# Kernel optimization log

Measured on AMD Instinct MI355X. Metric: run time of the kernel, lower is better.

The kernel has to match this reference:

```python
import jax, jax.numpy as jnp
import numpy as np

B, S, D = 16, 4096, 64
DROPOUT_KEY = jax.random.key(1)


def setup_inputs() -> dict:
    key = jax.random.key(0)
    kq, kk, kv = jax.random.split(key, 3)
    return {
        "query": jax.random.normal(kq, (B, S, D), dtype=jnp.float32),
        "key": jax.random.normal(kk, (B, S, D), dtype=jnp.float32),
        "value": jax.random.normal(kv, (B, S, D), dtype=jnp.float32),
        "dropout_p": jnp.float32(0.01),
        "inv_scale_factor": jnp.float32(8.0),  # sqrt(head_dim)
    }


def reference(query, key, value, dropout_p, inv_scale_factor):
    # scores: [B, Sq, Skv]
    scores = jnp.einsum("bqd,bkd->bqk", query, key) / inv_scale_factor
    attn = jax.nn.softmax(scores, axis=-1)
    # deterministic dropout with a fixed key (faithful train-mode dropout)
    keep = jax.random.bernoulli(DROPOUT_KEY, 1.0 - dropout_p, attn.shape)
    attn = jnp.where(keep, attn / (1.0 - dropout_p), 0.0)
    return jnp.einsum("bqk,bkd->bqd", attn, value)
```

## Files before the change

kernel.cpp:

```cpp
#include <hip/hip_runtime.h>
#include <stdint.h>


typedef _Float16 half4 __attribute__((ext_vector_type(4)));
typedef _Float16 half8 __attribute__((ext_vector_type(8)));
typedef float    f32x4 __attribute__((ext_vector_type(4)));

#if defined(__has_builtin)
#if __has_builtin(__builtin_amdgcn_exp2f)
#define EXP2(x) __builtin_amdgcn_exp2f(x)
#else
#define EXP2(x) exp2f(x)
#endif
#else
#define EXP2(x) exp2f(x)
#endif

#define ROTL(x, r) __builtin_amdgcn_alignbit((x), (x), 32 - (r))

__device__ __forceinline__ uint32_t tf2x32_xor(uint32_t n) {
  const uint32_t ks2 = 0x1BD11BDBu;
  uint32_t x0 = 0u, x1 = n;
#define TFR(r) { x0 += x1; x1 = ROTL(x1, r); x1 ^= x0; }
  x1 += 1u;
  TFR(13) TFR(15) TFR(26) TFR(6)
  x0 += 1u;  x1 += ks2 + 1u;
  TFR(17) TFR(29) TFR(16) TFR(24)
  x0 += ks2; x1 += 2u;
  TFR(13) TFR(15) TFR(26) TFR(6)
  x1 += 4u;
  TFR(17) TFR(29) TFR(16) TFR(24)
  x0 += 1u;  x1 += ks2 + 4u;
  TFR(13) TFR(15) TFR(26) TFR(6)
  x0 += ks2; x1 += 5u;
#undef TFR
  return x0 ^ x1;
}


__global__ void cvt_qk_kernel(const float* __restrict__ q,
                              const float* __restrict__ k,
                              const float* __restrict__ inv_scale,
                              _Float16* __restrict__ qh,
                              _Float16* __restrict__ kh) {
  const int tid = blockIdx.x * 256 + threadIdx.x;
  const int half_t = 1048576;
  const float qs = 1.4426950408889634f / inv_scale[0];
  if (tid < half_t) {
    float4 d = *(const float4*)(q + (size_t)tid * 4);
    half4 h = { (_Float16)(d.x * qs), (_Float16)(d.y * qs),
                (_Float16)(d.z * qs), (_Float16)(d.w * qs) };
    *(half4*)(qh + (size_t)tid * 4) = h;
  } else {
    const int t2 = tid - half_t;
    float4 d = *(const float4*)(k + (size_t)t2 * 4);
    half4 h = { (_Float16)d.x, (_Float16)d.y, (_Float16)d.z, (_Float16)d.w };
    *(half4*)(kh + (size_t)t2 * 4) = h;
  }
}

__global__ void cvt_v_kernel(const float* __restrict__ v,
                             _Float16* __restrict__ vt) {
  __shared__ float tile[64][65];
  const int b  = blockIdx.x >> 6;
  const int st = blockIdx.x & 63;
  const int t  = threadIdx.x;
  const float* src = v + ((size_t)b * 4096 + (size_t)st * 64) * 64;
#pragma unroll
  for (int i = 0; i < 4; ++i) {
    const int r = i * 16 + (t >> 4);
    const int c = (t & 15) * 4;
    float4 d = *(const float4*)(src + r * 64 + c);
    tile[r][c] = d.x; tile[r][c + 1] = d.y; tile[r][c + 2] = d.z; tile[r][c + 3] = d.w;
  }
  __syncthreads();
  _Float16* dst = vt + (size_t)b * 64 * 4096 + (size_t)st * 64;
#pragma unroll
  for (int i = 0; i < 4; ++i) {
    const int d0 = i * 16 + (t >> 4);
    const int s0 = (t & 15) * 4;
    half4 h = { (_Float16)tile[s0][d0],     (_Float16)tile[s0 + 1][d0],
                (_Float16)tile[s0 + 2][d0], (_Float16)tile[s0 + 3][d0] };
    *(half4*)(dst + (size_t)d0 * 4096 + s0) = h;
  }
}

__global__ __launch_bounds__(256, 4) void flash_attn(
    const _Float16* __restrict__ qh,
    const _Float16* __restrict__ kh,
    const _Float16* __restrict__ vth,
    const float* __restrict__ dropout_p,
    float* __restrict__ out) {
  __shared__ alignas(16) _Float16 Kt[2][64 * 72];
  __shared__ alignas(16) _Float16 Vt[2][64 * 72];

  const int pair = blockIdx.x & 7;
  const int q0   = (blockIdx.x >> 3) * 32;
  const int wave = threadIdx.x >> 6;
  const int lane = threadIdx.x & 63;
  const int l15  = lane & 15;
  const int l4   = lane >> 4;
  const int b2   = wave & 1;
  const int qw   = (wave >> 1) * 16;
  const int batch = pair + 8 * b2;

  const float keep_p = 1.0f - dropout_p[0];
  const uint32_t thr = (uint32_t)ceilf(keep_p * 8388608.0f);
  const uint32_t thr9 = (thr >= 8388608u) ? 0xFFFFFFFFu : (thr << 9);

  const _Float16* qp = qh +
      (((size_t)batch * 4096 + q0 + qw + l15) * 64 + l4 * 8);
  const half8 qfrag0 = *(const half8*)qp;
  const half8 qfrag1 = *(const half8*)(qp + 32);

  const f32x4 Zv = {0.f, 0.f, 0.f, 0.f};
  f32x4 oacc[4] = {Zv, Zv, Zv, Zv};
  float lpart = 0.f;

  const uint32_t nlo = ((uint32_t)batch << 24) +
                       ((uint32_t)(q0 + qw + l15) << 12) +
                       (uint32_t)(4 * l4);

  for (int step = 0; step < 64; ++step) {
    const int key0 = step * 64;
    __syncthreads();
#pragma unroll
    for (int bb = 0; bb < 2; ++bb) {
      const _Float16* kb = kh + ((size_t)(pair + 8 * bb) * 4096 + key0) * 64;
      const _Float16* vb = vth + (size_t)(pair + 8 * bb) * 64 * 4096 + key0;
#pragma unroll
      for (int i = 0; i < 2; ++i) {
        const int chunk = threadIdx.x + i * 256;
        const int row = chunk >> 3;
        const int c   = (chunk & 7) * 8;
        *(half8*)&Kt[bb][row * 72 + c] = *(const half8*)(kb + row * 64 + c);
        *(half8*)&Vt[bb][row * 72 + c] = *(const half8*)(vb + (size_t)row * 4096 + c);
      }
    }
    __syncthreads();

    f32x4 sacc[4];
#pragma unroll
    for (int t = 0; t < 4; ++t) {
      const half8 kf0 = *(const half8*)&Kt[b2][(16 * t + l15) * 72 + l4 * 8];
      const half8 kf1 = *(const half8*)&Kt[b2][(16 * t + l15) * 72 + l4 * 8 + 32];
      sacc[t] = __builtin_amdgcn_mfma_f32_16x16x32_f16(kf0, qfrag0, Zv, 0, 0, 0);
      sacc[t] = __builtin_amdgcn_mfma_f32_16x16x32_f16(kf1, qfrag1, sacc[t], 0, 0, 0);
    }

#pragma unroll
    for (int t = 0; t < 4; ++t) {
      const uint32_t cb = nlo + (uint32_t)(key0 + 16 * t);
      half4 pf;
#pragma unroll
      for (int r = 0; r < 4; ++r) {
        const uint32_t w = tf2x32_xor(cb + (uint32_t)r);
        const float p = EXP2(sacc[t][r]);
        lpart += p;
        pf[r] = (_Float16)((w < thr9) ? p : 0.0f);
      }
#pragma unroll
      for (int t2 = 0; t2 < 4; ++t2) {
        const half4 vf = *(const half4*)&Vt[b2][(16 * t2 + l15) * 72 + 16 * t + 4 * l4];
        oacc[t2] = __builtin_amdgcn_mfma_f32_16x16x16f16(pf, vf, oacc[t2], 0, 0, 0);
      }
    }
  }

  float l = lpart;
  l += __shfl_xor(l, 16, 64);
  l += __shfl_xor(l, 32, 64);
  float inv[4];
#pragma unroll
  for (int r = 0; r < 4; ++r)
    inv[r] = 1.0f / (keep_p * __shfl(l, 4 * l4 + r, 64));
#pragma unroll
  for (int t2 = 0; t2 < 4; ++t2)
#pragma unroll
    for (int r = 0; r < 4; ++r)
      out[((size_t)batch * 4096 + q0 + qw + 4 * l4 + r) * 64 + 16 * t2 + l15] =
          oacc[t2][r] * inv[r];
}


extern "C" void kernel_launch(void* const* d_in, const int* in_sizes, int n_in,
                              void* d_out, int out_size, void* d_ws, size_t ws_size,
                              hipStream_t stream) {
  const float* q   = (const float*)d_in[0];
  const float* k   = (const float*)d_in[1];
  const float* v   = (const float*)d_in[2];
  const float* dp  = (const float*)d_in[3];
  const float* isf = (const float*)d_in[4];
  float* out = (float*)d_out;

  const size_t N = (size_t)16 * 4096 * 64;
  _Float16* qh  = (_Float16*)d_ws;
  _Float16* kh  = qh + N;
  _Float16* vth = kh + N;

  cvt_qk_kernel<<<8192, 256, 0, stream>>>(q, k, isf, qh, kh);
  cvt_v_kernel<<<1024, 256, 0, stream>>>(v, vth);
  flash_attn<<<1024, 256, 0, stream>>>(qh, kh, vth, dp, out);
}
```

Before: 625.6 us.

## Precompute dropout mask as bitmask in separate kernel, read bits in attention

Adds a separate kernel that evaluates the Threefry hash once per attention element and packs keep decisions into 64-bit ballot words, 32 MB in total. The attention kernel then reads one mask word per row and step and applies it with shift and AND instead of running the hash inline. The hash also drops its first, trivial round. A fused fallback is kept for when the workspace is too small. The trade is extra mask memory traffic and one more kernel launch against removing hash ALU work from the MFMA loop.

```diff
diff --git a/kernel.cpp b/kernel.cpp
--- a/kernel.cpp
+++ b/kernel.cpp
@@ -18,12 +18,12 @@
 
 #define ROTL(x, r) __builtin_amdgcn_alignbit((x), (x), 32 - (r))
 
-__device__ __forceinline__ uint32_t tf2x32_xor(uint32_t n) {
+__device__ __forceinline__ uint32_t tf_hash(uint32_t x1) {
   const uint32_t ks2 = 0x1BD11BDBu;
-  uint32_t x0 = 0u, x1 = n;
+  uint32_t x0 = x1;
 #define TFR(r) { x0 += x1; x1 = ROTL(x1, r); x1 ^= x0; }
-  x1 += 1u;
-  TFR(13) TFR(15) TFR(26) TFR(6)
+  x1 = ROTL(x1, 13); x1 ^= x0;
+  TFR(15) TFR(26) TFR(6)
   x0 += 1u;  x1 += ks2 + 1u;
   TFR(17) TFR(29) TFR(16) TFR(24)
   x0 += ks2; x1 += 2u;
@@ -35,6 +35,38 @@
   x0 += ks2; x1 += 5u;
 #undef TFR
   return x0 ^ x1;
+}
+
+__device__ __forceinline__ uint32_t tf2x32_xor(uint32_t n) {
+  return tf_hash(n + 1u);
+}
+
+__device__ __forceinline__ uint32_t thr9_from(float keep_p) {
+  const uint32_t thr = (uint32_t)ceilf(keep_p * 8388608.0f);
+  return (thr >= 8388608u) ? 0xFFFFFFFFu : (thr << 9);
+}
+
+__global__ __launch_bounds__(256, 8) void prng_mask_kernel(
+    const float* __restrict__ dropout_p,
+    uint64_t* __restrict__ mask) {
+  const int lane = threadIdx.x & 63;
+  const uint32_t wid = (uint32_t)((blockIdx.x * 256 + threadIdx.x) >> 6);
+  const uint32_t thr9 = thr9_from(1.0f - dropout_p[0]);
+
+  const uint32_t base0 = (uint32_t)lane + 1u;
+  for (int it = 0; it < 128; ++it) {
+    const uint32_t g  = wid * 128u + (uint32_t)it;
+    const uint32_t nb = g * 256u + base0;
+    unsigned long long b0, b1, b2, b3;
+    b0 = __ballot(tf_hash(nb)         < thr9);
+    b1 = __ballot(tf_hash(nb + 64u)   < thr9);
+    b2 = __ballot(tf_hash(nb + 128u)  < thr9);
+    b3 = __ballot(tf_hash(nb + 192u)  < thr9);
+    if (lane == 0) {
+      uint64_t* p = mask + (size_t)g * 4;
+      p[0] = b0; p[1] = b1; p[2] = b2; p[3] = b3;
+    }
+  }
 }
 
 
@@ -89,6 +121,7 @@
     const _Float16* __restrict__ qh,
     const _Float16* __restrict__ kh,
     const _Float16* __restrict__ vth,
+    const uint64_t* __restrict__ mask,
     const float* __restrict__ dropout_p,
     float* __restrict__ out) {
   __shared__ alignas(16) _Float16 Kt[2][64 * 72];
@@ -103,26 +136,31 @@
   const int b2   = wave & 1;
   const int qw   = (wave >> 1) * 16;
   const int batch = pair + 8 * b2;
+  const int qrow  = q0 + qw + l15;
 
   const float keep_p = 1.0f - dropout_p[0];
-  const uint32_t thr = (uint32_t)ceilf(keep_p * 8388608.0f);
-  const uint32_t thr9 = (thr >= 8388608u) ? 0xFFFFFFFFu : (thr << 9);
-
-  const _Float16* qp = qh +
-      (((size_t)batch * 4096 + q0 + qw + l15) * 64 + l4 * 8);
+
+  const _Float16* qp = qh + (((size_t)batch * 4096 + qrow) * 64 + l4 * 8);
   const half8 qfrag0 = *(const half8*)qp;
   const half8 qfrag1 = *(const half8*)(qp + 32);
+
+  const uint64_t* mrow = mask + (((size_t)batch << 18) + ((size_t)qrow << 6));
+
+  int shl[2][4];
+#pragma unroll
+  for (int tt = 0; tt < 2; ++tt)
+#pragma unroll
+    for (int r = 0; r < 4; ++r) shl[tt][r] = 31 - 16 * tt - 4 * l4 - r;
 
   const f32x4 Zv = {0.f, 0.f, 0.f, 0.f};
   f32x4 oacc[4] = {Zv, Zv, Zv, Zv};
   float lpart = 0.f;
 
-  const uint32_t nlo = ((uint32_t)batch << 24) +
-                       ((uint32_t)(q0 + qw + l15) << 12) +
-                       (uint32_t)(4 * l4);
-
   for (int step = 0; step < 64; ++step) {
     const int key0 = step * 64;
+    const uint64_t mword = mrow[step];
+    const uint32_t mlo = (uint32_t)mword;
+    const uint32_t mhi = (uint32_t)(mword >> 32);
     __syncthreads();
 #pragma unroll
     for (int bb = 0; bb < 2; ++bb) {
@@ -150,6 +188,90 @@
 
 #pragma unroll
     for (int t = 0; t < 4; ++t) {
+      const uint32_t mh = (t & 2) ? mhi : mlo;
+      half4 pf;
+#pragma unroll
+      for (int r = 0; r < 4; ++r) {
+        const float p = EXP2(sacc[t][r]);
+        lpart += p;
+        const uint32_t km = (uint32_t)(((int32_t)(mh << shl[t & 1][r])) >> 31);
+        pf[r] = (_Float16)__uint_as_float(__float_as_uint(p) & km);
+      }
+#pragma unroll
+      for (int t2 = 0; t2 < 4; ++t2) {
+        const half4 vf = *(const half4*)&Vt[b2][(16 * t2 + l15) * 72 + 16 * t + 4 * l4];
+        oacc[t2] = __builtin_amdgcn_mfma_f32_16x16x16f16(pf, vf, oacc[t2], 0, 0, 0);
+      }
+    }
+  }
+
+  float l = lpart;
+  l += __shfl_xor(l, 16, 64);
+  l += __shfl_xor(l, 32, 64);
+  float inv[4];
+#pragma unroll
+  for (int r = 0; r < 4; ++r)
+    inv[r] = 1.0f / (keep_p * __shfl(l, 4 * l4 + r, 64));
+#pragma unroll
+  for (int t2 = 0; t2 < 4; ++t2)
+#pragma unroll
+    for (int r = 0; r < 4; ++r)
+      out[((size_t)batch * 4096 + q0 + qw + 4 * l4 + r) * 64 + 16 * t2 + l15] =
+          oacc[t2][r] * inv[r];
+}
+
+__global__ __launch_bounds__(256, 4) void flash_attn_fused(
+    const _Float16* __restrict__ qh, const _Float16* __restrict__ kh,
+    const _Float16* __restrict__ vth, const float* __restrict__ dropout_p,
+    float* __restrict__ out) {
+  __shared__ alignas(16) _Float16 Kt[2][64 * 72];
+  __shared__ alignas(16) _Float16 Vt[2][64 * 72];
+  const int pair = blockIdx.x & 7;
+  const int q0   = (blockIdx.x >> 3) * 32;
+  const int wave = threadIdx.x >> 6;
+  const int lane = threadIdx.x & 63;
+  const int l15  = lane & 15;
+  const int l4   = lane >> 4;
+  const int b2   = wave & 1;
+  const int qw   = (wave >> 1) * 16;
+  const int batch = pair + 8 * b2;
+  const float keep_p = 1.0f - dropout_p[0];
+  const uint32_t thr9 = thr9_from(keep_p);
+  const _Float16* qp = qh + (((size_t)batch * 4096 + q0 + qw + l15) * 64 + l4 * 8);
+  const half8 qfrag0 = *(const half8*)qp;
+  const half8 qfrag1 = *(const half8*)(qp + 32);
+  const f32x4 Zv = {0.f, 0.f, 0.f, 0.f};
+  f32x4 oacc[4] = {Zv, Zv, Zv, Zv};
+  float lpart = 0.f;
+  const uint32_t nlo = ((uint32_t)batch << 24) +
+                       ((uint32_t)(q0 + qw + l15) << 12) + (uint32_t)(4 * l4);
+  for (int step = 0; step < 64; ++step) {
+    const int key0 = step * 64;
+    __syncthreads();
+#pragma unroll
+    for (int bb = 0; bb < 2; ++bb) {
+      const _Float16* kb = kh + ((size_t)(pair + 8 * bb) * 4096 + key0) * 64;
+      const _Float16* vb = vth + (size_t)(pair + 8 * bb) * 64 * 4096 + key0;
+#pragma unroll
+      for (int i = 0; i < 2; ++i) {
+        const int chunk = threadIdx.x + i * 256;
+        const int row = chunk >> 3;
+        const int c   = (chunk & 7) * 8;
+        *(half8*)&Kt[bb][row * 72 + c] = *(const half8*)(kb + row * 64 + c);
+        *(half8*)&Vt[bb][row * 72 + c] = *(const half8*)(vb + (size_t)row * 4096 + c);
+      }
+    }
+    __syncthreads();
+    f32x4 sacc[4];
+#pragma unroll
+    for (int t = 0; t < 4; ++t) {
+      const half8 kf0 = *(const half8*)&Kt[b2][(16 * t + l15) * 72 + l4 * 8];
+      const half8 kf1 = *(const half8*)&Kt[b2][(16 * t + l15) * 72 + l4 * 8 + 32];
+      sacc[t] = __builtin_amdgcn_mfma_f32_16x16x32_f16(kf0, qfrag0, Zv, 0, 0, 0);
+      sacc[t] = __builtin_amdgcn_mfma_f32_16x16x32_f16(kf1, qfrag1, sacc[t], 0, 0, 0);
+    }
+#pragma unroll
+    for (int t = 0; t < 4; ++t) {
       const uint32_t cb = nlo + (uint32_t)(key0 + 16 * t);
       half4 pf;
 #pragma unroll
@@ -166,7 +288,6 @@
       }
     }
   }
-
   float l = lpart;
   l += __shfl_xor(l, 16, 64);
   l += __shfl_xor(l, 32, 64);
@@ -197,8 +318,15 @@
   _Float16* qh  = (_Float16*)d_ws;
   _Float16* kh  = qh + N;
   _Float16* vth = kh + N;
+  uint64_t* mask = (uint64_t*)((char*)d_ws + 3 * N * sizeof(_Float16));
+  const size_t need = 3 * N * sizeof(_Float16) + ((size_t)1 << 25);
 
   cvt_qk_kernel<<<8192, 256, 0, stream>>>(q, k, isf, qh, kh);
   cvt_v_kernel<<<1024, 256, 0, stream>>>(v, vth);
-  flash_attn<<<1024, 256, 0, stream>>>(qh, kh, vth, dp, out);
-}
+  if (ws_size >= need) {
+    prng_mask_kernel<<<2048, 256, 0, stream>>>(dp, mask);
+    flash_attn<<<1024, 256, 0, stream>>>(qh, kh, vth, mask, dp, out);
+  } else {
+    flash_attn_fused<<<1024, 256, 0, stream>>>(qh, kh, vth, dp, out);
+  }
+}
```

New measurement: 850.9 us. 1.36x slower.

## Map one batch per block and double-buffer K/V tiles with one barrier

Applied to the files above, without the earlier changes.

Each block now covers 64 queries of a single batch, so all four waves share one K/V tile instead of two waves per batch. This halves the global-to-LDS staging per block. The K/V tiles are double-buffered: the next tile is loaded while the current one is consumed, which removes the second __syncthreads per step. The first threefry round is also simplified using the known zero initial word, saving a few ALU ops in the dropout RNG.

```diff
diff --git a/kernel.cpp b/kernel.cpp
--- a/kernel.cpp
+++ b/kernel.cpp
@@ -20,10 +20,11 @@
 
 __device__ __forceinline__ uint32_t tf2x32_xor(uint32_t n) {
   const uint32_t ks2 = 0x1BD11BDBu;
-  uint32_t x0 = 0u, x1 = n;
+  uint32_t x1 = n + 1u;
+  uint32_t x0 = x1;
 #define TFR(r) { x0 += x1; x1 = ROTL(x1, r); x1 ^= x0; }
-  x1 += 1u;
-  TFR(13) TFR(15) TFR(26) TFR(6)
+  x1 = ROTL(x1, 13); x1 ^= x0;
+  TFR(15) TFR(26) TFR(6)
   x0 += 1u;  x1 += ks2 + 1u;
   TFR(17) TFR(29) TFR(16) TFR(24)
   x0 += ks2; x1 += 2u;
@@ -35,6 +36,11 @@
   x0 += ks2; x1 += 5u;
 #undef TFR
   return x0 ^ x1;
+}
+
+__device__ __forceinline__ uint32_t thr9_from(float keep_p) {
+  const uint32_t thr = (uint32_t)ceilf(keep_p * 8388608.0f);
+  return (thr >= 8388608u) ? 0xFFFFFFFFu : (thr << 9);
 }
 
 
@@ -94,22 +100,23 @@
   __shared__ alignas(16) _Float16 Kt[2][64 * 72];
   __shared__ alignas(16) _Float16 Vt[2][64 * 72];
 
-  const int pair = blockIdx.x & 7;
-  const int q0   = (blockIdx.x >> 3) * 32;
-  const int wave = threadIdx.x >> 6;
-  const int lane = threadIdx.x & 63;
-  const int l15  = lane & 15;
-  const int l4   = lane >> 4;
-  const int b2   = wave & 1;
-  const int qw   = (wave >> 1) * 16;
-  const int batch = pair + 8 * b2;
+  const int batch = blockIdx.x & 15;
+  const int q0    = (blockIdx.x >> 4) * 64;
+  const int wave  = threadIdx.x >> 6;
+  const int lane  = threadIdx.x & 63;
+  const int l15   = lane & 15;
+  const int l4    = lane >> 4;
+  const int qrow  = q0 + 16 * wave + l15;
 
   const float keep_p = 1.0f - dropout_p[0];
-  const uint32_t thr = (uint32_t)ceilf(keep_p * 8388608.0f);
-  const uint32_t thr9 = (thr >= 8388608u) ? 0xFFFFFFFFu : (thr << 9);
-
-  const _Float16* qp = qh +
-      (((size_t)batch * 4096 + q0 + qw + l15) * 64 + l4 * 8);
+  const uint32_t thr9 = thr9_from(keep_p);
+
+  const _Float16* kb = kh + (size_t)batch * 4096 * 64;
+  const _Float16* vb = vth + (size_t)batch * 64 * 4096;
+  const int srow = threadIdx.x >> 3;
+  const int sc   = (threadIdx.x & 7) * 8;
+
+  const _Float16* qp = qh + (((size_t)batch * 4096 + qrow) * 64 + l4 * 8);
   const half8 qfrag0 = *(const half8*)qp;
   const half8 qfrag1 = *(const half8*)(qp + 32);
 
@@ -117,33 +124,38 @@
   f32x4 oacc[4] = {Zv, Zv, Zv, Zv};
   float lpart = 0.f;
 
-  const uint32_t nlo = ((uint32_t)batch << 24) +
-                       ((uint32_t)(q0 + qw + l15) << 12) +
+  const uint32_t nlo = ((uint32_t)batch << 24) + ((uint32_t)qrow << 12) +
                        (uint32_t)(4 * l4);
 
+#pragma unroll
+  for (int i = 0; i < 2; ++i) {
+    const int row = srow + i * 32;
+    *(half8*)&Kt[0][row * 72 + sc] = *(const half8*)(kb + row * 64 + sc);
+    *(half8*)&Vt[0][row * 72 + sc] = *(const half8*)(vb + (size_t)row * 4096 + sc);
+  }
+
   for (int step = 0; step < 64; ++step) {
+    const int buf  = step & 1;
     const int key0 = step * 64;
     __syncthreads();
-#pragma unroll
-    for (int bb = 0; bb < 2; ++bb) {
-      const _Float16* kb = kh + ((size_t)(pair + 8 * bb) * 4096 + key0) * 64;
-      const _Float16* vb = vth + (size_t)(pair + 8 * bb) * 64 * 4096 + key0;
+
+    if (step < 63) {
+      const int nk = key0 + 64;
 #pragma unroll
       for (int i = 0; i < 2; ++i) {
-        const int chunk = threadIdx.x + i * 256;
-        const int row = chunk >> 3;
-        const int c   = (chunk & 7) * 8;
-        *(half8*)&Kt[bb][row * 72 + c] = *(const half8*)(kb + row * 64 + c);
-        *(half8*)&Vt[bb][row * 72 + c] = *(const half8*)(vb + (size_t)row * 4096 + c);
+        const int row = srow + i * 32;
+        *(half8*)&Kt[buf ^ 1][row * 72 + sc] =
+            *(const half8*)(kb + (size_t)(nk + row) * 64 + sc);
+        *(half8*)&Vt[buf ^ 1][row * 72 + sc] =
+            *(const half8*)(vb + (size_t)row * 4096 + nk + sc);
       }
     }
-    __syncthreads();
 
     f32x4 sacc[4];
 #pragma unroll
     for (int t = 0; t < 4; ++t) {
-      const half8 kf0 = *(const half8*)&Kt[b2][(16 * t + l15) * 72 + l4 * 8];
-      const half8 kf1 = *(const half8*)&Kt[b2][(16 * t + l15) * 72 + l4 * 8 + 32];
+      const half8 kf0 = *(const half8*)&Kt[buf][(16 * t + l15) * 72 + l4 * 8];
+      const half8 kf1 = *(const half8*)&Kt[buf][(16 * t + l15) * 72 + l4 * 8 + 32];
       sacc[t] = __builtin_amdgcn_mfma_f32_16x16x32_f16(kf0, qfrag0, Zv, 0, 0, 0);
       sacc[t] = __builtin_amdgcn_mfma_f32_16x16x32_f16(kf1, qfrag1, sacc[t], 0, 0, 0);
     }
@@ -161,7 +173,7 @@
       }
 #pragma unroll
       for (int t2 = 0; t2 < 4; ++t2) {
-        const half4 vf = *(const half4*)&Vt[b2][(16 * t2 + l15) * 72 + 16 * t + 4 * l4];
+        const half4 vf = *(const half4*)&Vt[buf][(16 * t2 + l15) * 72 + 16 * t + 4 * l4];
         oacc[t2] = __builtin_amdgcn_mfma_f32_16x16x16f16(pf, vf, oacc[t2], 0, 0, 0);
       }
     }
@@ -178,8 +190,8 @@
   for (int t2 = 0; t2 < 4; ++t2)
 #pragma unroll
     for (int r = 0; r < 4; ++r)
-      out[((size_t)batch * 4096 + q0 + qw + 4 * l4 + r) * 64 + 16 * t2 + l15] =
-          oacc[t2][r] * inv[r];
+      out[((size_t)batch * 4096 + q0 + 16 * wave + 4 * l4 + r) * 64 +
+          16 * t2 + l15] = oacc[t2][r] * inv[r];
 }
 
 
```

Result: no change. 628.2 us (+0.4%).
